# Kernel tuning notes

Measured on AMD Instinct MI355X. Metric: run time of the kernel, lower is better.

Reference implementation:

```python
import jax, jax.numpy as jnp
import numpy as np

B, L, H, E, V, X = 128, 1024, 256, 128, 50000, 100


def setup_inputs() -> dict:
    key = jax.random.key(0)
    ks = jax.random.split(key, 24)
    s = 0.02
    n = lambda k, shp: jax.random.normal(k, shp, dtype=jnp.float32) * s
    inp = {
        "y_t": jax.random.randint(ks[0], (B,), 0, V),
        "h0": n(ks[1], (B, H)),
        "c0": n(ks[2], (B, H)),
        "enc_outs": jax.random.normal(ks[3], (B, L, 2 * H), dtype=jnp.float32),
        "enc_feats": jax.random.normal(ks[4], (B * L, 2 * H), dtype=jnp.float32),
        "enc_padding_mask": jnp.ones((B, L), dtype=jnp.float32),
        "c_t_1": n(ks[5], (B, 2 * H)),
        "extra_zeros": jnp.zeros((B, X), dtype=jnp.float32),
        "enc_batch_extend_vocab": jax.random.randint(ks[6], (B, L), 0, V + X),
        "coverage": jnp.zeros((B, L), dtype=jnp.float32),
        # learned parameters (torch Linear convention: y = x @ W.T + b)
        "embed_W": n(ks[7], (V, E)),
        "Wih": n(ks[8], (4 * H, E)),
        "Whh": n(ks[9], (4 * H, H)),
        "bih": jnp.zeros((4 * H,), jnp.float32),
        "bhh": jnp.zeros((4 * H,), jnp.float32),
        "xctx_W": n(ks[10], (E, 2 * H + E)),
        "xctx_b": jnp.zeros((E,), jnp.float32),
        "Ws_W": n(ks[11], (2 * H, 2 * H)),
        "Ws_b": jnp.zeros((2 * H,), jnp.float32),
        "Wc_W": n(ks[12], (2 * H, 1)),
        "v_W": n(ks[13], (1, 2 * H)),
        "pgen_W": n(ks[14], (1, 4 * H + E)),
        "pgen_b": jnp.zeros((1,), jnp.float32),
        "proj_W": n(ks[15], (H, 3 * H)),
        "proj_b": jnp.zeros((H,), jnp.float32),
        "out_W": n(ks[16], (V, H)),
        "out_b": jnp.zeros((V,), jnp.float32),
    }
    return inp


def reference(y_t, h0, c0, enc_outs, enc_feats, enc_padding_mask, c_t_1,
              extra_zeros, enc_batch_extend_vocab, coverage,
              embed_W, Wih, Whh, bih, bhh, xctx_W, xctx_b, Ws_W, Ws_b,
              Wc_W, v_W, pgen_W, pgen_b, proj_W, proj_b, out_W, out_b):
    b, l = coverage.shape
    hd = h0.shape[1]
    # embedding + input-feeding context projection
    emb = embed_W[y_t]                                        # [B,E]
    x = jnp.concatenate([c_t_1, emb], axis=1) @ xctx_W.T + xctx_b  # [B,E]
    # single LSTM step (torch gate order i,f,g,o)
    gates = x @ Wih.T + bih + h0 @ Whh.T + bhh                # [B,4H]
    i_g, f_g, g_g, o_g = jnp.split(gates, 4, axis=1)
    c = jax.nn.sigmoid(f_g) * c0 + jax.nn.sigmoid(i_g) * jnp.tanh(g_g)
    h = jax.nn.sigmoid(o_g) * jnp.tanh(c)
    s_t_hat = jnp.concatenate([h, c], axis=1)                 # [B,2H]
    # coverage attention
    dec_feats = s_t_hat @ Ws_W.T + Ws_b                       # [B,2H]
    cov_feats = coverage.reshape(-1, 1) @ Wc_W.T              # [B*L,2H]
    feats = (enc_feats.reshape(b, l, 2 * hd)
             + dec_feats[:, None, :]
             + cov_feats.reshape(b, l, 2 * hd))
    energy = jnp.tanh(feats) @ v_W[0]                         # [B,L]
    a = jax.nn.softmax(energy, axis=1) * enc_padding_mask
    a = a / jnp.sum(a, axis=1, keepdims=True)
    c_t = jnp.einsum('bl,bld->bd', a, enc_outs)               # [B,2H]
    coverage_next = coverage + a
    # generation probability
    p_gen = jax.nn.sigmoid(
        jnp.concatenate([c_t, s_t_hat, x], axis=1) @ pgen_W.T + pgen_b)  # [B,1]
    # vocab distribution
    out_hid = jnp.concatenate([h, c_t], axis=1) @ proj_W.T + proj_b      # [B,H]
    logits = out_hid @ out_W.T + out_b                                    # [B,V]
    vocab_dist = p_gen * jax.nn.softmax(logits, axis=1)
    attn_dist_ = (1.0 - p_gen) * a
    # extended vocab + pointer scatter-add
    vd_ext = jnp.concatenate([vocab_dist, extra_zeros], axis=1)          # [B,V+X]
    rows = jnp.arange(b)[:, None]
    final_dist = vd_ext.at[rows, enc_batch_extend_vocab].add(attn_dist_)
    return (final_dist, h, c, c_t, a, p_gen, coverage_next)
```

## Files before the change

kernel.cpp:

```cpp
#include <hip/hip_runtime.h>
#include <hip/hip_bf16.h>
#include <cstdint>
#include <cstddef>

#define B_   128
#define L_   1024
#define H_   256
#define E_   128
#define V_   50000
#define X_   100
#define VX_  50100
#define LSTR 50112

#define OUT_H    6412800
#define OUT_C    6445568
#define OUT_CT   6478336
#define OUT_A    6543872
#define OUT_PGEN 6674944
#define OUT_COV  6675072

typedef __attribute__((ext_vector_type(8))) short bf16x8;
typedef __attribute__((ext_vector_type(4))) float f32x4;
typedef __attribute__((ext_vector_type(8))) unsigned short u16x8;

__device__ inline float bf2f(unsigned short u){
  union { unsigned int i; float f; } v; v.i = ((unsigned int)u) << 16; return v.f;
}
__device__ inline unsigned short f2bf(float f){
  union { float f; unsigned int i; } v; v.f = f;
  unsigned int lsb = (v.i >> 16) & 1u;
  v.i += 0x7fffu + lsb;
  return (unsigned short)(v.i >> 16);
}
__device__ inline float sigm(float x){ return __builtin_amdgcn_rcpf(1.f + __expf(-x)); }
__device__ inline float tanh_f(float x){
  float ax = fabsf(x);
  float t  = __expf(-2.f * ax);
  float r  = (1.f - t) * __builtin_amdgcn_rcpf(1.f + t);
  return copysignf(r, x);
}
__device__ inline bool is_f32m(const void* mask){
  return ((const unsigned short*)mask)[0] != 0x3F80u;
}
__device__ inline float ldf(const void* p, size_t i, bool f32){
  return f32 ? ((const float*)p)[i] : bf2f(((const unsigned short*)p)[i]);
}
__device__ inline void stf(void* p, size_t i, float v, bool f32){
  if (f32) ((float*)p)[i] = v; else ((unsigned short*)p)[i] = f2bf(v);
}
__device__ inline void atomic_add_bf16(unsigned short* addr, float val){
  uintptr_t a = (uintptr_t)addr;
  unsigned int* word = (unsigned int*)(a & ~(uintptr_t)3);
  bool hi = (a & 2) != 0;
  unsigned int old = *word, assumed;
  do {
    assumed = old;
    unsigned short cur = hi ? (unsigned short)(assumed >> 16) : (unsigned short)(assumed & 0xffffu);
    unsigned short nv = f2bf(bf2f(cur) + val);
    unsigned int next = hi ? ((assumed & 0x0000ffffu) | ((unsigned int)nv << 16))
                           : ((assumed & 0xffff0000u) | (unsigned int)nv);
    old = atomicCAS(word, assumed, next);
  } while (old != assumed);
}

__global__ void k_pre(const void* __restrict__ xctx_W, const void* __restrict__ Wih,
                      const void* __restrict__ Whh, const void* __restrict__ Ws_W,
                      const void* __restrict__ proj_W, const void* __restrict__ bih,
                      const void* __restrict__ bhh, const void* __restrict__ mask,
                      float* __restrict__ xctxT, float* __restrict__ gatesT,
                      float* __restrict__ bg, float* __restrict__ WsT,
                      float* __restrict__ projT){
  bool f32 = is_f32m(mask);
  const int total = 81920 + 131072 + 262144 + 262144 + 196608 + 1024;
  for (int e = blockIdx.x * 256 + threadIdx.x; e < total; e += gridDim.x * 256){
    int r = e;
    if (r < 81920){
      int n = r / 640, k = r - n * 640;
      xctxT[k * 128 + n] = ldf(xctx_W, r, f32);
    } else if ((r -= 81920) < 131072){
      int n = r >> 7, k = r & 127;
      gatesT[k * 1024 + n] = ldf(Wih, r, f32);
    } else if ((r -= 131072) < 262144){
      int n = r >> 8, k = r & 255;
      gatesT[(128 + k) * 1024 + n] = ldf(Whh, r, f32);
    } else if ((r -= 262144) < 262144){
      int n = r >> 9, k = r & 511;
      WsT[k * 512 + n] = ldf(Ws_W, r, f32);
    } else if ((r -= 262144) < 196608){
      int n = r / 768, k = r - n * 768;
      projT[k * 256 + n] = ldf(proj_W, r, f32);
    } else {
      r -= 196608;
      bg[r] = ldf(bih, r, f32) + ldf(bhh, r, f32);
    }
  }
}

__global__ void kA_row(const int* __restrict__ y_t, const void* __restrict__ c_t_1,
                       const void* __restrict__ embed_W, const void* __restrict__ h0,
                       const void* __restrict__ c0, const float* __restrict__ xctxT,
                       const void* __restrict__ xctx_b, const float* __restrict__ gatesT,
                       const float* __restrict__ bg, const float* __restrict__ WsT,
                       const void* __restrict__ Ws_b, const void* __restrict__ mask,
                       float* __restrict__ x_ws, float* __restrict__ st_ws,
                       float* __restrict__ dec_ws, void* __restrict__ out){
  bool f32 = is_f32m(mask);
  __shared__ float act[768];
  int m = blockIdx.x, t = threadIdx.x;
  act[t]       = ldf(c_t_1, (size_t)m * 512 + t, f32);
  act[256 + t] = ldf(c_t_1, (size_t)m * 512 + 256 + t, f32);
  if (t < 128){
    size_t em = (size_t)y_t[m] * 128;
    act[512 + t] = ldf(embed_W, em + t, f32);
  }
  __syncthreads();
  float xv = 0.f;
  if (t < 128){
    xv = ldf(xctx_b, t, f32);
    for (int k = 0; k < 640; ++k) xv += act[k] * xctxT[k * 128 + t];
  }
  __syncthreads();
  if (t < 128){ act[t] = xv; x_ws[m * 128 + t] = xv; }
  act[128 + t] = ldf(h0, (size_t)m * 256 + t, f32);
  __syncthreads();
  float g[4];
  #pragma unroll
  for (int gi = 0; gi < 4; ++gi) g[gi] = bg[t + gi * 256];
  for (int k = 0; k < 384; ++k){
    float a = act[k];
    const float* wr = gatesT + (size_t)k * 1024 + t;
    #pragma unroll
    for (int gi = 0; gi < 4; ++gi) g[gi] += a * wr[gi * 256];
  }
  float c0v = ldf(c0, (size_t)m * 256 + t, f32);
  float c = sigm(g[1]) * c0v + sigm(g[0]) * tanh_f(g[2]);
  float h = sigm(g[3]) * tanh_f(c);
  st_ws[m * 512 + t]       = h;
  st_ws[m * 512 + 256 + t] = c;
  stf(out, (size_t)OUT_H + m * 256 + t, h, f32);
  stf(out, (size_t)OUT_C + m * 256 + t, c, f32);
  __syncthreads();
  act[t] = h; act[256 + t] = c;
  __syncthreads();
  float a0 = ldf(Ws_b, t, f32), a1 = ldf(Ws_b, t + 256, f32);
  for (int k = 0; k < 512; ++k){
    float a = act[k];
    const float* wr = WsT + (size_t)k * 512 + t;
    a0 += a * wr[0];
    a1 += a * wr[256];
  }
  dec_ws[m * 512 + t]       = a0;
  dec_ws[m * 512 + 256 + t] = a1;
}

__global__ void k4_energy(const void* __restrict__ enc_feats, const float* __restrict__ dec_ws,
                          const void* __restrict__ coverage, const void* __restrict__ Wc,
                          const void* __restrict__ vW, const void* __restrict__ mask,
                          float* __restrict__ energy_ws){
  bool f32 = is_f32m(mask);
  int g = blockIdx.x * 4 + (threadIdx.x >> 6);
  int lane = threadIdx.x & 63;
  int b = g >> 10;
  int d0 = lane * 8;
  float vv[8], wc[8], ef[8];
  if (f32){
    const float* vp = (const float*)vW + d0;
    const float* wp = (const float*)Wc + d0;
    const float* ep = (const float*)enc_feats + (size_t)g * 512 + d0;
    float4 a0 = ((const float4*)vp)[0], a1 = ((const float4*)vp)[1];
    float4 b0 = ((const float4*)wp)[0], b1 = ((const float4*)wp)[1];
    float4 c0 = ((const float4*)ep)[0], c1 = ((const float4*)ep)[1];
    vv[0]=a0.x; vv[1]=a0.y; vv[2]=a0.z; vv[3]=a0.w; vv[4]=a1.x; vv[5]=a1.y; vv[6]=a1.z; vv[7]=a1.w;
    wc[0]=b0.x; wc[1]=b0.y; wc[2]=b0.z; wc[3]=b0.w; wc[4]=b1.x; wc[5]=b1.y; wc[6]=b1.z; wc[7]=b1.w;
    ef[0]=c0.x; ef[1]=c0.y; ef[2]=c0.z; ef[3]=c0.w; ef[4]=c1.x; ef[5]=c1.y; ef[6]=c1.z; ef[7]=c1.w;
  } else {
    u16x8 a = *(const u16x8*)((const unsigned short*)vW + d0);
    u16x8 w = *(const u16x8*)((const unsigned short*)Wc + d0);
    u16x8 e = *(const u16x8*)((const unsigned short*)enc_feats + (size_t)g * 512 + d0);
    #pragma unroll
    for (int jj = 0; jj < 8; ++jj){ vv[jj] = bf2f(a[jj]); wc[jj] = bf2f(w[jj]); ef[jj] = bf2f(e[jj]); }
  }
  const float4* dr = (const float4*)(dec_ws + b * 512 + d0);
  float4 dv0 = dr[0], dv1 = dr[1];
  float dec[8] = {dv0.x, dv0.y, dv0.z, dv0.w, dv1.x, dv1.y, dv1.z, dv1.w};
  float cov = ldf(coverage, g, f32);
  float acc = 0.f;
  #pragma unroll
  for (int jj = 0; jj < 8; ++jj){
    float f = ef[jj] + dec[jj] + cov * wc[jj];
    acc += tanh_f(f) * vv[jj];
  }
  #pragma unroll
  for (int off = 32; off > 0; off >>= 1) acc += __shfl_down(acc, off, 64);
  if (lane == 0) energy_ws[g] = acc;
}

__global__ void k5_attn(const float* __restrict__ energy_ws, const void* __restrict__ mask,
                        const void* __restrict__ coverage,
                        float* __restrict__ a_ws, float* __restrict__ ct_ws, void* __restrict__ out){
  bool f32 = is_f32m(mask);
  __shared__ float red[256];
  int b = blockIdx.x, t = threadIdx.x;
  const float* er = energy_ws + b * 1024;
  float e[4];
  float mx = -1e30f;
  #pragma unroll
  for (int i = 0; i < 4; ++i){ e[i] = er[t + i * 256]; mx = fmaxf(mx, e[i]); }
  red[t] = mx; __syncthreads();
  for (int s = 128; s > 0; s >>= 1){ if (t < s) red[t] = fmaxf(red[t], red[t + s]); __syncthreads(); }
  float M = red[0]; __syncthreads();
  float sum = 0.f;
  #pragma unroll
  for (int i = 0; i < 4; ++i){
    float mk = ldf(mask, (size_t)b * 1024 + t + i * 256, f32);
    e[i] = __expf(e[i] - M) * mk;
    sum += e[i];
  }
  red[t] = sum; __syncthreads();
  for (int s = 128; s > 0; s >>= 1){ if (t < s) red[t] += red[t + s]; __syncthreads(); }
  float inv = 1.f / red[0];
  #pragma unroll
  for (int i = 0; i < 4; ++i){
    int l = t + i * 256;
    float av = e[i] * inv;
    a_ws[b * 1024 + l] = av;
    stf(out, (size_t)OUT_A + b * 1024 + l, av, f32);
    stf(out, (size_t)OUT_COV + b * 1024 + l, ldf(coverage, (size_t)b * 1024 + l, f32) + av, f32);
  }
  ct_ws[b * 512 + t] = 0.f;
  ct_ws[b * 512 + t + 256] = 0.f;
}

__global__ void k6_ctx(const float* __restrict__ a_ws, const void* __restrict__ enc_outs,
                       const void* __restrict__ mask, float* __restrict__ ct_ws){
  bool f32 = is_f32m(mask);
  __shared__ float ash[256];
  int blk = blockIdx.x;
  int b = blk >> 2, part = blk & 3;
  int t = threadIdx.x;
  int l0 = part * 256;
  ash[t] = a_ws[b * 1024 + l0 + t];
  __syncthreads();
  int d = t * 2;
  float acc0 = 0.f, acc1 = 0.f;
  if (f32){
    const float* base = (const float*)enc_outs + ((size_t)(b * 1024 + l0)) * 512 + d;
    for (int l = 0; l < 256; ++l){
      float2 v = *(const float2*)(base + (size_t)l * 512);
      float a = ash[l];
      acc0 += a * v.x; acc1 += a * v.y;
    }
  } else {
    const unsigned short* base = (const unsigned short*)enc_outs + ((size_t)(b * 1024 + l0)) * 512 + d;
    for (int l = 0; l < 256; ++l){
      unsigned int pk = *(const unsigned int*)(base + (size_t)l * 512);
      float a = ash[l];
      acc0 += a * bf2f((unsigned short)(pk & 0xffffu));
      acc1 += a * bf2f((unsigned short)(pk >> 16));
    }
  }
  atomicAdd(&ct_ws[b * 512 + d],     acc0);
  atomicAdd(&ct_ws[b * 512 + d + 1], acc1);
}

__global__ void kC_row(const float* __restrict__ ct_ws, const float* __restrict__ st_ws,
                       const float* __restrict__ x_ws, const void* __restrict__ pgen_W,
                       const void* __restrict__ pgen_b, const float* __restrict__ projT,
                       const void* __restrict__ proj_b, const void* __restrict__ mask,
                       float* __restrict__ pgen_ws, unsigned short* __restrict__ outhid_bf,
                       void* __restrict__ out){
  bool f32 = is_f32m(mask);
  __shared__ float act[768];
  int b = blockIdx.x, t = threadIdx.x;
  stf(out, (size_t)OUT_CT + b * 512 + t,       ct_ws[b * 512 + t], f32);
  stf(out, (size_t)OUT_CT + b * 512 + t + 256, ct_ws[b * 512 + t + 256], f32);
  float acc = 0.f;
  for (int k = t; k < 1152; k += 256){
    float v = (k < 512) ? ct_ws[b * 512 + k]
            : (k < 1024) ? st_ws[b * 512 + (k - 512)]
            : x_ws[b * 128 + (k - 1024)];
    acc += v * ldf(pgen_W, k, f32);
  }
  act[t] = acc; __syncthreads();
  for (int s = 128; s > 0; s >>= 1){ if (t < s) act[t] += act[t + s]; __syncthreads(); }
  if (t == 0){
    float p = sigm(act[0] + ldf(pgen_b, 0, f32));
    pgen_ws[b] = p;
    stf(out, (size_t)OUT_PGEN + b, p, f32);
  }
  __syncthreads();
  act[t]       = st_ws[b * 512 + t];
  act[256 + t] = ct_ws[b * 512 + t];
  act[512 + t] = ct_ws[b * 512 + 256 + t];
  __syncthreads();
  float oacc = ldf(proj_b, t, f32);
  for (int k = 0; k < 768; ++k) oacc += act[k] * projT[k * 256 + t];
  outhid_bf[b * 256 + t] = f2bf(oacc);
}

__global__ void k9_logits(const unsigned short* __restrict__ outhid_bf, const void* __restrict__ out_W,
                          const void* __restrict__ out_b, const void* __restrict__ mask,
                          unsigned short* __restrict__ logits_bf){
  bool f32 = is_f32m(mask);
  int wid = blockIdx.x * 4 + (threadIdx.x >> 6);
  if (wid >= V_ / 16) return;
  int lane = threadIdx.x & 63;
  int q = lane >> 4, r = lane & 15;
  int n0 = wid * 16;
  const bf16x8* Ar = (const bf16x8*)(outhid_bf);
  float bias = ldf(out_b, n0 + r, f32);
  f32x4 acc[8];
  #pragma unroll
  for (int mt = 0; mt < 8; ++mt) acc[mt] = (f32x4){0.f, 0.f, 0.f, 0.f};
  #pragma unroll
  for (int kk = 0; kk < 8; ++kk){
    bf16x8 bfrag;
    if (f32){
      const float* wf = (const float*)out_W + (size_t)(n0 + r) * 256 + kk * 32 + q * 8;
      float4 w0 = ((const float4*)wf)[0], w1 = ((const float4*)wf)[1];
      bfrag[0] = (short)f2bf(w0.x); bfrag[1] = (short)f2bf(w0.y);
      bfrag[2] = (short)f2bf(w0.z); bfrag[3] = (short)f2bf(w0.w);
      bfrag[4] = (short)f2bf(w1.x); bfrag[5] = (short)f2bf(w1.y);
      bfrag[6] = (short)f2bf(w1.z); bfrag[7] = (short)f2bf(w1.w);
    } else {
      bfrag = ((const bf16x8*)((const unsigned short*)out_W + (size_t)(n0 + r) * 256))[kk * 4 + q];
    }
    #pragma unroll
    for (int mt = 0; mt < 8; ++mt){
      bf16x8 afrag = Ar[(mt * 16 + r) * 32 + kk * 4 + q];
      acc[mt] = __builtin_amdgcn_mfma_f32_16x16x32_bf16(afrag, bfrag, acc[mt], 0, 0, 0);
    }
  }
  #pragma unroll
  for (int mt = 0; mt < 8; ++mt){
    #pragma unroll
    for (int rr = 0; rr < 4; ++rr){
      int m = mt * 16 + q * 4 + rr;
      logits_bf[(size_t)m * LSTR + n0 + r] = f2bf(acc[mt][rr] + bias);
    }
  }
}

__global__ void k10_rowred(const unsigned short* __restrict__ logits_bf, float* __restrict__ pm, float* __restrict__ ps){
  __shared__ float red[256];
  int blk = blockIdx.x;
  int b = blk >> 2, part = blk & 3;
  int t = threadIdx.x;
  const unsigned short* row = logits_bf + (size_t)b * LSTR + part * 12500;
  float mx = -1e30f;
  for (int c = t; c < 12500; c += 256) mx = fmaxf(mx, bf2f(row[c]));
  red[t] = mx; __syncthreads();
  for (int s = 128; s > 0; s >>= 1){ if (t < s) red[t] = fmaxf(red[t], red[t + s]); __syncthreads(); }
  float M = red[0]; __syncthreads();
  float sum = 0.f;
  for (int c = t; c < 12500; c += 256) sum += __expf(bf2f(row[c]) - M);
  red[t] = sum; __syncthreads();
  for (int s = 128; s > 0; s >>= 1){ if (t < s) red[t] += red[t + s]; __syncthreads(); }
  if (t == 0){ pm[blk] = M; ps[blk] = red[0]; }
}

__global__ void k11s_vocab_scatter(const unsigned short* __restrict__ logits_bf,
                                   const float* __restrict__ pm, const float* __restrict__ ps,
                                   const float* __restrict__ pgen_ws, const float* __restrict__ a_ws,
                                   const int* __restrict__ ebev, const void* __restrict__ mask,
                                   void* __restrict__ out){
  bool f32 = is_f32m(mask);
  int b = blockIdx.x, t = threadIdx.x;
  float M = fmaxf(fmaxf(pm[b * 4], pm[b * 4 + 1]), fmaxf(pm[b * 4 + 2], pm[b * 4 + 3]));
  float S = 0.f;
  #pragma unroll
  for (int p = 0; p < 4; ++p) S += ps[b * 4 + p] * __expf(pm[b * 4 + p] - M);
  float pg = pgen_ws[b];
  float Sc = pg / S;
  const unsigned short* lrow = logits_bf + (size_t)b * LSTR;
  for (int c0 = t * 8; c0 < VX_; c0 += 2048){
    #pragma unroll
    for (int j = 0; j < 8; ++j){
      int c = c0 + j;
      if (c < VX_){
        float v = (c < V_) ? __expf(bf2f(lrow[c]) - M) * Sc : 0.f;
        stf(out, (size_t)b * VX_ + c, v, f32);
      }
    }
  }
  __syncthreads();
  float q = 1.f - pg;
  #pragma unroll
  for (int i = 0; i < 4; ++i){
    int l = t + i * 256;
    int g = b * 1024 + l;
    float val = q * a_ws[g];
    size_t idx = (size_t)b * VX_ + ebev[g];
    if (f32) atomicAdd((float*)out + idx, val);
    else     atomic_add_bf16((unsigned short*)out + idx, val);
  }
}

extern "C" void kernel_launch(void* const* d_in, const int* in_sizes, int n_in,
                              void* d_out, int out_size, void* d_ws, size_t ws_size,
                              hipStream_t stream){
  const int*  y_t   = (const int*)d_in[0];
  const void* h0    = d_in[1];
  const void* c0    = d_in[2];
  const void* enc_outs  = d_in[3];
  const void* enc_feats = d_in[4];
  const void* mask  = d_in[5];
  const void* c_t_1 = d_in[6];
  const int*  ebev  = (const int*)d_in[8];
  const void* coverage = d_in[9];
  const void* embed_W = d_in[10];
  const void* Wih   = d_in[11];
  const void* Whh   = d_in[12];
  const void* bih   = d_in[13];
  const void* bhh   = d_in[14];
  const void* xctx_W = d_in[15];
  const void* xctx_b = d_in[16];
  const void* Ws_W  = d_in[17];
  const void* Ws_b  = d_in[18];
  const void* Wc_W  = d_in[19];
  const void* v_W   = d_in[20];
  const void* pgen_W = d_in[21];
  const void* pgen_b = d_in[22];
  const void* proj_W = d_in[23];
  const void* proj_b = d_in[24];
  const void* out_W = d_in[25];
  const void* out_b = d_in[26];

  float* ws        = (float*)d_ws;
  float* x_ws      = ws;
  float* st_ws     = ws + 16384;
  float* dec_ws    = ws + 81920;
  float* energy_ws = ws + 147456;
  float* a_ws      = ws + 278528;
  float* ct_ws     = ws + 409600;
  float* pgen_ws   = ws + 475136;
  float* pm_ws     = ws + 475264;
  float* ps_ws     = ws + 475776;
  unsigned short* outhid_bf = (unsigned short*)(ws + 476576);
  unsigned short* logits_bf = (unsigned short*)(ws + 492960);
  float* xctxT     = ws + 3700128;
  float* gatesT    = ws + 3782048;
  float* bg_ws     = ws + 4175264;
  float* WsT       = ws + 4176288;
  float* projT     = ws + 4438432;

  k_pre  <<<1024, 256, 0, stream>>>(xctx_W, Wih, Whh, Ws_W, proj_W, bih, bhh, mask,
                                    xctxT, gatesT, bg_ws, WsT, projT);
  kA_row <<<128, 256, 0, stream>>>(y_t, c_t_1, embed_W, h0, c0, xctxT, xctx_b,
                                   gatesT, bg_ws, WsT, Ws_b, mask,
                                   x_ws, st_ws, dec_ws, d_out);
  k4_energy<<<32768, 256, 0, stream>>>(enc_feats, dec_ws, coverage, Wc_W, v_W, mask, energy_ws);
  k5_attn<<<128, 256, 0, stream>>>(energy_ws, mask, coverage, a_ws, ct_ws, d_out);
  k6_ctx <<<512, 256, 0, stream>>>(a_ws, enc_outs, mask, ct_ws);
  kC_row <<<128, 256, 0, stream>>>(ct_ws, st_ws, x_ws, pgen_W, pgen_b, projT, proj_b,
                                   mask, pgen_ws, outhid_bf, d_out);
  k9_logits<<<(V_ / 16 + 3) / 4, 256, 0, stream>>>(outhid_bf, out_W, out_b, mask, logits_bf);
  k10_rowred<<<512, 256, 0, stream>>>(logits_bf, pm_ws, ps_ws);
  k11s_vocab_scatter<<<128, 256, 0, stream>>>(logits_bf, pm_ws, ps_ws, pgen_ws, a_ws,
                                              ebev, mask, d_out);
}
```

Baseline: 796.2 us.

## Rebalance energy, context and vocab kernels; split vocab write from pointer scatter

The energy kernel now runs as a persistent grid of 1024 blocks, where each wave loops over 32 positions and loads v_W and Wc only once. The context kernel splits L into 8 parts instead of 4, doubling the number of blocks. The vocab-softmax write is moved into a 2D grid with vectorized 8-wide loads and stores, and the pointer scatter-add becomes its own kernel. Together these aim to raise parallelism and cut per-block overhead in the memory-bound stages, at the cost of one extra launch and twice as many atomics on ct.

After: 765.3 us. 1.04x faster.

```diff
diff --git a/kernel.cpp b/kernel.cpp
--- a/kernel.cpp
+++ b/kernel.cpp
@@ -22,6 +22,7 @@
 typedef __attribute__((ext_vector_type(8))) short bf16x8;
 typedef __attribute__((ext_vector_type(4))) float f32x4;
 typedef __attribute__((ext_vector_type(8))) unsigned short u16x8;
+typedef __attribute__((ext_vector_type(4))) unsigned short u16x4;
 
 __device__ inline float bf2f(unsigned short u){
   union { unsigned int i; float f; } v; v.i = ((unsigned int)u) << 16; return v.f;
@@ -158,41 +159,49 @@
                           const void* __restrict__ vW, const void* __restrict__ mask,
                           float* __restrict__ energy_ws){
   bool f32 = is_f32m(mask);
-  int g = blockIdx.x * 4 + (threadIdx.x >> 6);
+  int wave = blockIdx.x * 4 + (threadIdx.x >> 6);
   int lane = threadIdx.x & 63;
-  int b = g >> 10;
   int d0 = lane * 8;
-  float vv[8], wc[8], ef[8];
+  float vv[8], wc[8];
   if (f32){
-    const float* vp = (const float*)vW + d0;
-    const float* wp = (const float*)Wc + d0;
-    const float* ep = (const float*)enc_feats + (size_t)g * 512 + d0;
-    float4 a0 = ((const float4*)vp)[0], a1 = ((const float4*)vp)[1];
-    float4 b0 = ((const float4*)wp)[0], b1 = ((const float4*)wp)[1];
-    float4 c0 = ((const float4*)ep)[0], c1 = ((const float4*)ep)[1];
+    const float4* vp = (const float4*)((const float*)vW + d0);
+    const float4* wp = (const float4*)((const float*)Wc + d0);
+    float4 a0 = vp[0], a1 = vp[1], b0 = wp[0], b1 = wp[1];
     vv[0]=a0.x; vv[1]=a0.y; vv[2]=a0.z; vv[3]=a0.w; vv[4]=a1.x; vv[5]=a1.y; vv[6]=a1.z; vv[7]=a1.w;
     wc[0]=b0.x; wc[1]=b0.y; wc[2]=b0.z; wc[3]=b0.w; wc[4]=b1.x; wc[5]=b1.y; wc[6]=b1.z; wc[7]=b1.w;
-    ef[0]=c0.x; ef[1]=c0.y; ef[2]=c0.z; ef[3]=c0.w; ef[4]=c1.x; ef[5]=c1.y; ef[6]=c1.z; ef[7]=c1.w;
   } else {
     u16x8 a = *(const u16x8*)((const unsigned short*)vW + d0);
     u16x8 w = *(const u16x8*)((const unsigned short*)Wc + d0);
-    u16x8 e = *(const u16x8*)((const unsigned short*)enc_feats + (size_t)g * 512 + d0);
-    #pragma unroll
-    for (int jj = 0; jj < 8; ++jj){ vv[jj] = bf2f(a[jj]); wc[jj] = bf2f(w[jj]); ef[jj] = bf2f(e[jj]); }
-  }
-  const float4* dr = (const float4*)(dec_ws + b * 512 + d0);
-  float4 dv0 = dr[0], dv1 = dr[1];
-  float dec[8] = {dv0.x, dv0.y, dv0.z, dv0.w, dv1.x, dv1.y, dv1.z, dv1.w};
-  float cov = ldf(coverage, g, f32);
-  float acc = 0.f;
-  #pragma unroll
-  for (int jj = 0; jj < 8; ++jj){
-    float f = ef[jj] + dec[jj] + cov * wc[jj];
-    acc += tanh_f(f) * vv[jj];
-  }
-  #pragma unroll
-  for (int off = 32; off > 0; off >>= 1) acc += __shfl_down(acc, off, 64);
-  if (lane == 0) energy_ws[g] = acc;
+    #pragma unroll
+    for (int jj = 0; jj < 8; ++jj){ vv[jj] = bf2f(a[jj]); wc[jj] = bf2f(w[jj]); }
+  }
+  for (int i = 0; i < 32; ++i){
+    int g = wave + 4096 * i;
+    int b = g >> 10;
+    float ef[8];
+    if (f32){
+      const float4* ep = (const float4*)((const float*)enc_feats + (size_t)g * 512 + d0);
+      float4 c0v = ep[0], c1v = ep[1];
+      ef[0]=c0v.x; ef[1]=c0v.y; ef[2]=c0v.z; ef[3]=c0v.w; ef[4]=c1v.x; ef[5]=c1v.y; ef[6]=c1v.z; ef[7]=c1v.w;
+    } else {
+      u16x8 e = *(const u16x8*)((const unsigned short*)enc_feats + (size_t)g * 512 + d0);
+      #pragma unroll
+      for (int jj = 0; jj < 8; ++jj) ef[jj] = bf2f(e[jj]);
+    }
+    const float4* dr = (const float4*)(dec_ws + b * 512 + d0);
+    float4 dv0 = dr[0], dv1 = dr[1];
+    float dec[8] = {dv0.x, dv0.y, dv0.z, dv0.w, dv1.x, dv1.y, dv1.z, dv1.w};
+    float cov = ldf(coverage, g, f32);
+    float acc = 0.f;
+    #pragma unroll
+    for (int jj = 0; jj < 8; ++jj){
+      float f = ef[jj] + dec[jj] + cov * wc[jj];
+      acc += tanh_f(f) * vv[jj];
+    }
+    #pragma unroll
+    for (int off = 32; off > 0; off >>= 1) acc += __shfl_down(acc, off, 64);
+    if (lane == 0) energy_ws[g] = acc;
+  }
 }
 
 __global__ void k5_attn(const float* __restrict__ energy_ws, const void* __restrict__ mask,
@@ -234,25 +243,25 @@
 __global__ void k6_ctx(const float* __restrict__ a_ws, const void* __restrict__ enc_outs,
                        const void* __restrict__ mask, float* __restrict__ ct_ws){
   bool f32 = is_f32m(mask);
-  __shared__ float ash[256];
+  __shared__ float ash[128];
   int blk = blockIdx.x;
-  int b = blk >> 2, part = blk & 3;
+  int b = blk >> 3, part = blk & 7;
   int t = threadIdx.x;
-  int l0 = part * 256;
-  ash[t] = a_ws[b * 1024 + l0 + t];
+  int l0 = part * 128;
+  if (t < 128) ash[t] = a_ws[b * 1024 + l0 + t];
   __syncthreads();
   int d = t * 2;
   float acc0 = 0.f, acc1 = 0.f;
   if (f32){
     const float* base = (const float*)enc_outs + ((size_t)(b * 1024 + l0)) * 512 + d;
-    for (int l = 0; l < 256; ++l){
+    for (int l = 0; l < 128; ++l){
       float2 v = *(const float2*)(base + (size_t)l * 512);
       float a = ash[l];
       acc0 += a * v.x; acc1 += a * v.y;
     }
   } else {
     const unsigned short* base = (const unsigned short*)enc_outs + ((size_t)(b * 1024 + l0)) * 512 + d;
-    for (int l = 0; l < 256; ++l){
+    for (int l = 0; l < 128; ++l){
       unsigned int pk = *(const unsigned int*)(base + (size_t)l * 512);
       float a = ash[l];
       acc0 += a * bf2f((unsigned short)(pk & 0xffffu));
@@ -359,21 +368,37 @@
   if (t == 0){ pm[blk] = M; ps[blk] = red[0]; }
 }
 
-__global__ void k11s_vocab_scatter(const unsigned short* __restrict__ logits_bf,
-                                   const float* __restrict__ pm, const float* __restrict__ ps,
-                                   const float* __restrict__ pgen_ws, const float* __restrict__ a_ws,
-                                   const int* __restrict__ ebev, const void* __restrict__ mask,
-                                   void* __restrict__ out){
-  bool f32 = is_f32m(mask);
-  int b = blockIdx.x, t = threadIdx.x;
+__global__ void k11_vocab(const unsigned short* __restrict__ logits_bf, const float* __restrict__ pm,
+                          const float* __restrict__ ps, const float* __restrict__ pgen_ws,
+                          const void* __restrict__ mask, void* __restrict__ out){
+  bool f32 = is_f32m(mask);
+  int b = blockIdx.y, t = threadIdx.x;
   float M = fmaxf(fmaxf(pm[b * 4], pm[b * 4 + 1]), fmaxf(pm[b * 4 + 2], pm[b * 4 + 3]));
   float S = 0.f;
   #pragma unroll
   for (int p = 0; p < 4; ++p) S += ps[b * 4 + p] * __expf(pm[b * 4 + p] - M);
-  float pg = pgen_ws[b];
-  float Sc = pg / S;
+  float Sc = pgen_ws[b] / S;
+  int c0 = blockIdx.x * 2048 + t * 8;
+  if (c0 >= VX_) return;
   const unsigned short* lrow = logits_bf + (size_t)b * LSTR;
-  for (int c0 = t * 8; c0 < VX_; c0 += 2048){
+  if (c0 + 8 <= V_){
+    u16x8 lv = *(const u16x8*)(lrow + c0);
+    float v[8];
+    #pragma unroll
+    for (int j = 0; j < 8; ++j) v[j] = __expf(bf2f(lv[j]) - M) * Sc;
+    size_t idx = (size_t)b * VX_ + c0;
+    if (f32){
+      float4* o = (float4*)((float*)out + idx);
+      o[0] = (float4){v[0], v[1], v[2], v[3]};
+      o[1] = (float4){v[4], v[5], v[6], v[7]};
+    } else {
+      u16x4* o = (u16x4*)((unsigned short*)out + idx);
+      u16x4 w0, w1;
+      #pragma unroll
+      for (int j = 0; j < 4; ++j){ w0[j] = f2bf(v[j]); w1[j] = f2bf(v[4 + j]); }
+      o[0] = w0; o[1] = w1;
+    }
+  } else {
     #pragma unroll
     for (int j = 0; j < 8; ++j){
       int c = c0 + j;
@@ -383,17 +408,18 @@
       }
     }
   }
-  __syncthreads();
-  float q = 1.f - pg;
-  #pragma unroll
-  for (int i = 0; i < 4; ++i){
-    int l = t + i * 256;
-    int g = b * 1024 + l;
-    float val = q * a_ws[g];
-    size_t idx = (size_t)b * VX_ + ebev[g];
-    if (f32) atomicAdd((float*)out + idx, val);
-    else     atomic_add_bf16((unsigned short*)out + idx, val);
-  }
+}
+
+__global__ void k12_scatter(const int* __restrict__ ebev, const float* __restrict__ a_ws,
+                            const float* __restrict__ pgen_ws, const void* __restrict__ mask,
+                            void* __restrict__ out){
+  bool f32 = is_f32m(mask);
+  int g = blockIdx.x * 256 + threadIdx.x;
+  int b = g >> 10;
+  float val = (1.f - pgen_ws[b]) * a_ws[g];
+  size_t idx = (size_t)b * VX_ + ebev[g];
+  if (f32) atomicAdd((float*)out + idx, val);
+  else     atomic_add_bf16((unsigned short*)out + idx, val);
 }
 
 extern "C" void kernel_launch(void* const* d_in, const int* in_sizes, int n_in,
@@ -449,13 +475,13 @@
   kA_row <<<128, 256, 0, stream>>>(y_t, c_t_1, embed_W, h0, c0, xctxT, xctx_b,
                                    gatesT, bg_ws, WsT, Ws_b, mask,
                                    x_ws, st_ws, dec_ws, d_out);
-  k4_energy<<<32768, 256, 0, stream>>>(enc_feats, dec_ws, coverage, Wc_W, v_W, mask, energy_ws);
+  k4_energy<<<1024, 256, 0, stream>>>(enc_feats, dec_ws, coverage, Wc_W, v_W, mask, energy_ws);
   k5_attn<<<128, 256, 0, stream>>>(energy_ws, mask, coverage, a_ws, ct_ws, d_out);
-  k6_ctx <<<512, 256, 0, stream>>>(a_ws, enc_outs, mask, ct_ws);
+  k6_ctx <<<1024, 256, 0, stream>>>(a_ws, enc_outs, mask, ct_ws);
   kC_row <<<128, 256, 0, stream>>>(ct_ws, st_ws, x_ws, pgen_W, pgen_b, projT, proj_b,
                                    mask, pgen_ws, outhid_bf, d_out);
   k9_logits<<<(V_ / 16 + 3) / 4, 256, 0, stream>>>(outhid_bf, out_W, out_b, mask, logits_bf);
   k10_rowred<<<512, 256, 0, stream>>>(logits_bf, pm_ws, ps_ws);
-  k11s_vocab_scatter<<<128, 256, 0, stream>>>(logits_bf, pm_ws, ps_ws, pgen_ws, a_ws,
-                                              ebev, mask, d_out);
-}
+  k11_vocab<<<dim3(25, 128), 256, 0, stream>>>(logits_bf, pm_ws, ps_ws, pgen_ws, mask, d_out);
+  k12_scatter<<<512, 256, 0, stream>>>(ebev, a_ws, pgen_ws, mask, d_out);
+}
```
